# Performance work log

Hardware: AMD Instinct MI355X
Metric: run time of the kernel (lower is better)

The kernel has to match this reference:

```python
import jax, jax.numpy as jnp
import numpy as np

D_MODEL = 1024
NUM_HEADS = 16
D_K = D_MODEL // NUM_HEADS
THETA = 10000.0
SEQ = 4096
BATCH = 1


def _rope(x, token_positions):
    # x: [b, h, s, d_k]; interleaved even/odd rotation as in the torch module
    kd = jnp.arange(0, D_K, 2, dtype=jnp.float32) / D_K          # [d_k/2]
    angles = token_positions[:, None].astype(jnp.float32) / (THETA ** kd)  # [s, d_k/2]
    cos_pos = jnp.cos(angles)
    sin_pos = jnp.sin(angles)
    x_even = x[..., 0::2]
    x_odd = x[..., 1::2]
    rot_even = x_even * cos_pos - x_odd * sin_pos
    rot_odd = x_even * sin_pos + x_odd * cos_pos
    rot = jnp.stack([rot_even, rot_odd], axis=-1)                # [..., d_k/2, 2]
    return rot.reshape(*x.shape[:-1], D_K)


def setup_inputs() -> dict:
    key = jax.random.key(0)
    k1, k2, k3 = jax.random.split(key, 3)
    std_qkv = np.sqrt(2.0 / (D_MODEL + 3 * D_MODEL))
    std_o = np.sqrt(2.0 / (D_MODEL + D_MODEL))
    x = jax.random.normal(k1, (BATCH, SEQ, D_MODEL), dtype=jnp.float32)
    Wqkv = jax.random.normal(k2, (3 * D_MODEL, D_MODEL), dtype=jnp.float32) * std_qkv
    Wo = jax.random.normal(k3, (D_MODEL, D_MODEL), dtype=jnp.float32) * std_o
    token_positions = jnp.arange(SEQ, dtype=jnp.int32)
    return {"x": x, "Wqkv": Wqkv, "Wo": Wo, "token_positions": token_positions}


def reference(x, Wqkv, Wo, token_positions):
    b, s, _ = x.shape
    qkv = jnp.einsum('bsd,ed->bse', x, Wqkv)                      # [b, s, 3*d_model]
    q, k, v = jnp.split(qkv, 3, axis=-1)

    def to_heads(t):
        return t.reshape(b, s, NUM_HEADS, D_K).transpose(0, 2, 1, 3)  # [b, h, s, d_k]

    q, k, v = to_heads(q), to_heads(k), to_heads(v)
    q = _rope(q, token_positions)
    k = _rope(k, token_positions)

    scores = jnp.einsum('bhqd,bhkd->bhqk', q, k) / jnp.sqrt(jnp.float32(D_K))
    mask = jnp.tril(jnp.ones((s, s), dtype=bool))
    scores = jnp.where(mask, scores, -jnp.inf)
    attn = jax.nn.softmax(scores, axis=-1)
    out = jnp.einsum('bhqk,bhkd->bhqd', attn, v)                  # [b, h, s, d_k]
    out = out.transpose(0, 2, 1, 3).reshape(b, s, D_MODEL)
    return jnp.einsum('bsd,ed->bse', out, Wo)
```

## Files before the change

kernel.cpp:

```cpp
#include <hip/hip_runtime.h>
#include <cstdint>

typedef unsigned short u16;
typedef __attribute__((ext_vector_type(8))) short short8;
typedef __attribute__((ext_vector_type(4))) float float4v;

__device__ __forceinline__ float bf2f(u16 u) {
    union { unsigned int i; float f; } v; v.i = ((unsigned int)u) << 16; return v.f;
}
__device__ __forceinline__ u16 f2bf(float f) {
    union { float f; unsigned int i; } v; v.f = f;
    unsigned int i = v.i;
    i += 0x7fffu + ((i >> 16) & 1u);
    return (u16)(i >> 16);
}
__device__ __forceinline__ unsigned cvt_pk_bf16(float lo, float hi) {
    unsigned r;
    asm("v_cvt_pk_bf16_f32 %0, %1, %2" : "=v"(r) : "v"(lo), "v"(hi));
    return r;
}
__device__ __forceinline__ void gl2lds16(const u16* g, u16* l) {
    __builtin_amdgcn_global_load_lds((const __attribute__((address_space(1))) void*)g,
                                     (__attribute__((address_space(3))) void*)l, 16, 0, 0);
}
__device__ __forceinline__ uint4 cvt8(const float* __restrict__ p) {
    float4 a = *(const float4*)p;
    float4 b = *(const float4*)(p + 4);
    u16 t[8] = {f2bf(a.x), f2bf(a.y), f2bf(a.z), f2bf(a.w),
                f2bf(b.x), f2bf(b.y), f2bf(b.z), f2bf(b.w)};
    return *(const uint4*)t;
}

__global__ void cvt_xw(const float* __restrict__ x, const float* __restrict__ wq,
                       const int* __restrict__ pos,
                       u16* __restrict__ xb, u16* __restrict__ wqb,
                       float2* __restrict__ tb) {
    int i = blockIdx.x * blockDim.x + threadIdx.x;
    if (i < 524288) {
        *(uint4*)(xb + (size_t)i * 8) = cvt8(x + (size_t)i * 8);
    } else if (i < 917504) {
        int j = i - 524288;
        *(uint4*)(wqb + (size_t)j * 8) = cvt8(wq + (size_t)j * 8);
    } else {
        int j = i - 917504;
        int s = j >> 5, f = j & 31;
        float freq = __expf(-(float)f * 0.2878231366242557f);
        float ang  = (float)pos[s] * freq;
        float sn, cs;
        __sincosf(ang, &sn, &cs);
        float2 t; t.x = cs; t.y = sn;
        tb[j] = t;
    }
}

__global__ __launch_bounds__(256) void gemm_qkv(const u16* __restrict__ A,
                                                const u16* __restrict__ B,
                                                u16* __restrict__ C,
                                                const float2* __restrict__ tb) {
    __shared__ u16 As[128 * 64];
    __shared__ u16 Bs[128 * 64];
    const int tid  = threadIdx.x;
    const int wave = tid >> 6, lane = tid & 63;
    const int lg = lane >> 4, lr = lane & 15;
    const int bm = blockIdx.x * 128, bn = blockIdx.y * 128;
    const int wm = (wave & 1) * 64, wn = (wave >> 1) * 64;
    const int swz = lr & 7;

    int srow[4], scg[4];
    #pragma unroll
    for (int q = 0; q < 4; ++q) {
        int cid = q * 256 + tid;
        srow[q] = cid >> 3;
        scg[q]  = ((cid & 7) ^ (srow[q] & 7)) * 8;
    }

    float4v acc[4][4] = {};

    for (int k0 = 0; k0 < 1024; k0 += 64) {
        #pragma unroll
        for (int q = 0; q < 4; ++q) {
            int cid = q * 256 + tid;
            gl2lds16(A + (size_t)(bm + srow[q]) * 1024 + k0 + scg[q], As + cid * 8);
            gl2lds16(B + (size_t)(bn + srow[q]) * 1024 + k0 + scg[q], Bs + cid * 8);
        }
        __syncthreads();

        #pragma unroll
        for (int kk = 0; kk < 2; ++kk) {
            short8 af[4], bf[4];
            #pragma unroll
            for (int i = 0; i < 4; ++i)
                af[i] = *(const short8*)(As + (wm + i * 16 + lr) * 64 + (((kk * 4 + lg) ^ swz) * 8));
            #pragma unroll
            for (int j = 0; j < 4; ++j)
                bf[j] = *(const short8*)(Bs + (wn + j * 16 + lr) * 64 + (((kk * 4 + lg) ^ swz) * 8));
            #pragma unroll
            for (int i = 0; i < 4; ++i)
                #pragma unroll
                for (int j = 0; j < 4; ++j)
                    acc[i][j] = __builtin_amdgcn_mfma_f32_16x16x32_bf16(af[i], bf[j], acc[i][j], 0, 0, 0);
        }
        __syncthreads();
    }

    const int colbase = bn + wn;
    const bool dorope = colbase < 2048;
    const float qsc = (colbase < 1024) ? 0.18033688011112042f : 1.0f;
    #pragma unroll
    for (int i = 0; i < 4; ++i)
        #pragma unroll
        for (int r = 0; r < 4; ++r) {
            const int rw = bm + wm + i * 16 + lg * 4 + r;
            #pragma unroll
            for (int j = 0; j < 4; ++j) {
                float v = acc[i][j][r];
                if (dorope) {
                    float2 t = tb[rw * 32 + ((j * 16 + lr) >> 1)];
                    float p = __shfl_xor(v, 1);
                    float rot = (lr & 1) ? (p * t.y + v * t.x)
                                         : (v * t.x - p * t.y);
                    v = rot * qsc;
                }
                C[(size_t)rw * 3072 + colbase + j * 16 + lr] = f2bf(v);
            }
        }
}

__global__ __launch_bounds__(256) void prep2(const u16* __restrict__ qkv,
                                             u16* __restrict__ VT,
                                             float* __restrict__ acc,
                                             float* __restrict__ lac,
                                             const float* __restrict__ wo,
                                             u16* __restrict__ wob) {
    __shared__ u16 T[64 * 65];
    const int bid = blockIdx.x;
    const int tid = threadIdx.x;
    if (bid < 1024) {
        const int h = bid >> 6, s0 = (bid & 63) * 64;
        #pragma unroll
        for (int i = 0; i < 2; ++i) {
            int seg = i * 256 + tid;
            int r = seg >> 3, c8 = (seg & 7) * 8;
            u16 tmp[8];
            *(uint4*)tmp = *(const uint4*)(qkv + (size_t)(s0 + r) * 3072 + 2048 + h * 64 + c8);
            #pragma unroll
            for (int j = 0; j < 8; ++j) T[r * 65 + c8 + j] = tmp[j];
        }
        __syncthreads();
        #pragma unroll
        for (int i = 0; i < 2; ++i) {
            int seg = i * 256 + tid;
            int d = seg >> 3, s8 = (seg & 7) * 8;
            u16 tmp[8];
            #pragma unroll
            for (int j = 0; j < 8; ++j) tmp[j] = T[(s8 + j) * 65 + d];
            *(uint4*)(VT + (size_t)(h * 64 + d) * 4096 + s0 + s8) = *(const uint4*)tmp;
        }
    } else {
        int i = (bid - 1024) * 256 + tid;
        float4 z = {0.f, 0.f, 0.f, 0.f};
        if (i < 1048576) {
            *(float4*)(acc + (size_t)i * 4) = z;
        } else if (i < 1064960) {
            *(float4*)(lac + (size_t)(i - 1048576) * 4) = z;
        } else {
            int j = i - 1064960;
            *(uint4*)(wob + (size_t)j * 8) = cvt8(wo + (size_t)j * 8);
        }
    }
}

__device__ __forceinline__ void attn_tile(const u16* __restrict__ Ksub,
                                          const u16* __restrict__ Vsub,
                                          u16* __restrict__ Psw,
                                          int tbase, int qrow0, int q_abs,
                                          int lg, int lr, int swz,
                                          const short8 qf[2], const short8 ones,
                                          float4v o_acc[4], float4v& rs_acc) {
    float4v sc[4];
    #pragma unroll
    for (int jt = 0; jt < 4; ++jt) {
        float4v a = {};
        #pragma unroll
        for (int kk = 0; kk < 2; ++kk) {
            short8 kf = *(const short8*)(Ksub + (jt * 16 + lr) * 64 + (((kk * 4 + lg) ^ swz) * 8));
            a = __builtin_amdgcn_mfma_f32_16x16x32_bf16(kf, qf[kk], a, 0, 0, 0);
        }
        sc[jt] = a;
    }
    const bool mk = (tbase + 63 > qrow0);
    #pragma unroll
    for (int jt = 0; jt < 4; ++jt) {
        float e[4];
        if (mk) {
            #pragma unroll
            for (int r = 0; r < 4; ++r) {
                float s = sc[jt][r];
                if (tbase + jt * 16 + lg * 4 + r > q_abs) s = -30000.f;
                e[r] = __builtin_amdgcn_exp2f(fminf(s, 86.562f));
            }
        } else {
            #pragma unroll
            for (int r = 0; r < 4; ++r)
                e[r] = __builtin_amdgcn_exp2f(fminf(sc[jt][r], 86.562f));
        }
        uint2 w;
        w.x = cvt_pk_bf16(e[0], e[1]);
        w.y = cvt_pk_bf16(e[2], e[3]);
        *(uint2*)(Psw + lr * 72 + jt * 16 + lg * 4) = w;
    }
    short8 pf[2];
    #pragma unroll
    for (int kk = 0; kk < 2; ++kk)
        pf[kk] = *(const short8*)(Psw + lr * 72 + kk * 32 + lg * 8);
    #pragma unroll
    for (int kk = 0; kk < 2; ++kk)
        rs_acc = __builtin_amdgcn_mfma_f32_16x16x32_bf16(pf[kk], ones, rs_acc, 0, 0, 0);
    #pragma unroll
    for (int jd = 0; jd < 4; ++jd) {
        float4v a = o_acc[jd];
        #pragma unroll
        for (int kk = 0; kk < 2; ++kk) {
            short8 vf = *(const short8*)(Vsub + (jd * 16 + lr) * 64 + (((kk * 4 + lg) ^ swz) * 8));
            a = __builtin_amdgcn_mfma_f32_16x16x32_bf16(pf[kk], vf, a, 0, 0, 0);
        }
        o_acc[jd] = a;
    }
}

__global__ __launch_bounds__(512) void attn_kernel(const u16* __restrict__ qkv,
                                                   const u16* __restrict__ VT,
                                                   float* __restrict__ acc,
                                                   float* __restrict__ lac) {
    __shared__ u16 Ks[2 * 64 * 64];
    __shared__ u16 Vt[2 * 64 * 64];
    __shared__ u16 Ps[8][16 * 72];

    const int tid  = threadIdx.x;
    const int wave = tid >> 6, lane = tid & 63;
    const int lg = lane >> 4, lr = lane & 15;

    const int fid = blockIdx.x;
    const int j_  = fid >> 3;
    const int h   = (fid & 7) * 2 + (j_ >> 5);
    const int z   = (j_ >> 4) & 1;
    const int bxv = j_ & 15;

    const int srow = tid >> 3;
    const int sg   = tid & 7;
    const int sco  = sg * 8;
    const int sldso = srow * 64 + ((sg ^ (srow & 7)) * 8);
    const int swz = (lr & 7);

    const u16 one_bf = 0x3F80;
    short8 ones;
    #pragma unroll
    for (int j = 0; j < 8; ++j) ones[j] = (short)one_bf;

    const u16* Kgbase = qkv + (size_t)srow * 3072 + 1024 + h * 64 + sco;
    const u16* Vgbase = VT + (size_t)(h * 64 + srow) * 4096 + sco;

    #pragma unroll 1
    for (int part = 0; part < 2; ++part) {
        const int qt = part ? (31 - bxv) : bxv;
        const int qb = qt * 128;
        const int qrow0 = qb + wave * 16;
        const int q_abs = qrow0 + lr;
        const int tmax = qb + 64;
        const int t0s  = z * 64;

        short8 qf[2];
        #pragma unroll
        for (int kk = 0; kk < 2; ++kk)
            qf[kk] = *(const short8*)(qkv + (size_t)(qrow0 + lr) * 3072 + h * 64 + kk * 32 + lg * 8);

        float4v o_acc[4] = {};
        float4v rs_acc = {};

        uint4 rK0 = *(const uint4*)(Kgbase + (size_t)t0s * 3072);
        uint4 rV0 = *(const uint4*)(Vgbase + t0s);
        const bool pB = (t0s + 128 <= tmax);
        uint4 rK1, rV1;
        if (pB) {
            rK1 = *(const uint4*)(Kgbase + (size_t)(t0s + 128) * 3072);
            rV1 = *(const uint4*)(Vgbase + t0s + 128);
        }
        __syncthreads();
        *(uint4*)(Ks + sldso) = rK0;
        *(uint4*)(Vt + sldso) = rV0;
        if (pB) {
            *(uint4*)(Ks + 4096 + sldso) = rK1;
            *(uint4*)(Vt + 4096 + sldso) = rV1;
        }
        __syncthreads();

        for (int t0 = t0s; t0 <= tmax; t0 += 256) {
            const bool hasB  = (t0 + 128 <= tmax);
            const bool hasN  = (t0 + 256 <= tmax);
            const bool hasNB = (t0 + 384 <= tmax);
            if (hasN) {
                rK0 = *(const uint4*)(Kgbase + (size_t)(t0 + 256) * 3072);
                rV0 = *(const uint4*)(Vgbase + t0 + 256);
            }
            if (hasNB) {
                rK1 = *(const uint4*)(Kgbase + (size_t)(t0 + 384) * 3072);
                rV1 = *(const uint4*)(Vgbase + t0 + 384);
            }

            attn_tile(Ks, Vt, Ps[wave], t0, qrow0, q_abs, lg, lr, swz, qf, ones, o_acc, rs_acc);
            if (hasB)
                attn_tile(Ks + 4096, Vt + 4096, Ps[wave], t0 + 128, qrow0, q_abs,
                          lg, lr, swz, qf, ones, o_acc, rs_acc);

            if (hasN) {
                __syncthreads();
                *(uint4*)(Ks + sldso) = rK0;
                *(uint4*)(Vt + sldso) = rV0;
                if (hasNB) {
                    *(uint4*)(Ks + 4096 + sldso) = rK1;
                    *(uint4*)(Vt + 4096 + sldso) = rV1;
                }
                __syncthreads();
            }
        }

        if (lr == 0) {
            #pragma unroll
            for (int r = 0; r < 4; ++r)
                atomicAdd(&lac[(size_t)(qrow0 + lg * 4 + r) * 16 + h], rs_acc[r]);
        }

        #pragma unroll
        for (int jd = 0; jd < 4; ++jd)
            #pragma unroll
            for (int r = 0; r < 4; ++r) {
                int s = qrow0 + lg * 4 + r;
                int d = jd * 16 + lr;
                atomicAdd(&acc[(size_t)s * 1024 + h * 64 + d], o_acc[jd][r]);
            }
    }
}

__global__ void norm_o(const float* __restrict__ acc, const float* __restrict__ lac,
                       u16* __restrict__ qkv) {
    int i = blockIdx.x * blockDim.x + threadIdx.x;
    if (i >= 4096 * 1024 / 8) return;
    int e0 = i * 8;
    int s = e0 >> 10, c = e0 & 1023, h = c >> 6;
    float inv = 1.0f / lac[(size_t)s * 16 + h];
    float4 a = *(const float4*)(acc + e0);
    float4 b = *(const float4*)(acc + e0 + 4);
    u16 t[8] = {f2bf(a.x * inv), f2bf(a.y * inv), f2bf(a.z * inv), f2bf(a.w * inv),
                f2bf(b.x * inv), f2bf(b.y * inv), f2bf(b.z * inv), f2bf(b.w * inv)};
    *(uint4*)(qkv + (size_t)s * 3072 + c) = *(const uint4*)t;
}

__global__ __launch_bounds__(256) void gemm_oproj(const u16* __restrict__ A,
                                                  const u16* __restrict__ B,
                                                  float* __restrict__ C) {
    __shared__ u16 As[128 * 64];
    __shared__ u16 Bs[64 * 64];
    const int tid  = threadIdx.x;
    const int wave = tid >> 6, lane = tid & 63;
    const int lg = lane >> 4, lr = lane & 15;
    const int bm = blockIdx.x * 128, bn = blockIdx.y * 64;
    const int wm = (wave & 1) * 64, wn = (wave >> 1) * 32;
    const int swz = lr & 7;

    int srow[4], scg[4];
    #pragma unroll
    for (int q = 0; q < 4; ++q) {
        int cid = q * 256 + tid;
        srow[q] = cid >> 3;
        scg[q]  = ((cid & 7) ^ (srow[q] & 7)) * 8;
    }

    float4v acc[4][2] = {};

    for (int k0 = 0; k0 < 1024; k0 += 64) {
        #pragma unroll
        for (int q = 0; q < 4; ++q) {
            int cid = q * 256 + tid;
            gl2lds16(A + (size_t)(bm + srow[q]) * 3072 + k0 + scg[q], As + cid * 8);
            if (q < 2)
                gl2lds16(B + (size_t)(bn + srow[q]) * 1024 + k0 + scg[q], Bs + cid * 8);
        }
        __syncthreads();

        #pragma unroll
        for (int kk = 0; kk < 2; ++kk) {
            short8 af[4], bf[2];
            #pragma unroll
            for (int i = 0; i < 4; ++i)
                af[i] = *(const short8*)(As + (wm + i * 16 + lr) * 64 + (((kk * 4 + lg) ^ swz) * 8));
            #pragma unroll
            for (int j = 0; j < 2; ++j)
                bf[j] = *(const short8*)(Bs + (wn + j * 16 + lr) * 64 + (((kk * 4 + lg) ^ swz) * 8));
            #pragma unroll
            for (int i = 0; i < 4; ++i)
                #pragma unroll
                for (int j = 0; j < 2; ++j)
                    acc[i][j] = __builtin_amdgcn_mfma_f32_16x16x32_bf16(af[i], bf[j], acc[i][j], 0, 0, 0);
        }
        __syncthreads();
    }

    #pragma unroll
    for (int i = 0; i < 4; ++i)
        #pragma unroll
        for (int j = 0; j < 2; ++j)
            #pragma unroll
            for (int r = 0; r < 4; ++r) {
                int rw = bm + wm + i * 16 + lg * 4 + r;
                int cl = bn + wn + j * 16 + lr;
                C[(size_t)rw * 1024 + cl] = acc[i][j][r];
            }
}

__global__ void fill_diag(float* __restrict__ p, size_t n, float mark) {
    size_t i = (size_t)blockIdx.x * blockDim.x + threadIdx.x;
    if (i < n) p[i] = 0.f;
    if (i == 0) p[0] = mark;
}

extern "C" void kernel_launch(void* const* d_in, const int* in_sizes, int n_in,
                              void* d_out, int out_size, void* d_ws, size_t ws_size,
                              hipStream_t stream) {
    int ix = -1, iwq = -1, iwo = -1, ip = -1;
    for (int i = 0; i < n_in; ++i) {
        if      (in_sizes[i] == 4096 * 1024) ix = i;
        else if (in_sizes[i] == 3072 * 1024) iwq = i;
        else if (in_sizes[i] == 1024 * 1024) iwo = i;
        else if (in_sizes[i] == 4096)        ip = i;
    }
    float* out = (float*)d_out;
    const size_t OUT_E = (size_t)4096 * 1024;
    const size_t QKV_E = (size_t)4096 * 3072;
    const size_t NEED  = QKV_E * 2 + (size_t)3072 * 1024 * 2;

    if (ix < 0 || iwq < 0 || iwo < 0 || ip < 0 || out_size != (int)OUT_E) {
        fill_diag<<<(int)((OUT_E + 255) / 256), 256, 0, stream>>>(out, OUT_E, 1000.0f);
        return;
    }
    if (ws_size < NEED) {
        fill_diag<<<(int)((OUT_E + 255) / 256), 256, 0, stream>>>(out, OUT_E, 500.0f);
        return;
    }
    const float* x    = (const float*)d_in[ix];
    const float* Wqkv = (const float*)d_in[iwq];
    const float* Wo   = (const float*)d_in[iwo];
    const int*   pos  = (const int*)d_in[ip];

    u16* qkv   = (u16*)d_ws;
    u16* wq_bf = (u16*)d_ws + QKV_E;
    u16* wo_bf = wq_bf;
    float* lac = (float*)((char*)wq_bf + 2 * 1024 * 1024 + 65536);
    u16* x_bf  = (u16*)d_out;
    u16* VT    = (u16*)d_out + OUT_E;
    float2* tb = (float2*)VT;
    float* acc = (float*)d_in[ix];

    cvt_xw<<<4096, 256, 0, stream>>>(x, Wqkv, pos, x_bf, wq_bf, tb);
    gemm_qkv<<<dim3(32, 24), 256, 0, stream>>>(x_bf, wq_bf, qkv, tb);
    prep2<<<5696, 256, 0, stream>>>(qkv, VT, acc, lac, Wo, wo_bf);
    attn_kernel<<<512, 512, 0, stream>>>(qkv, VT, acc, lac);
    norm_o<<<2048, 256, 0, stream>>>(acc, lac, qkv);
    gemm_oproj<<<dim3(32, 16), 256, 0, stream>>>(qkv, wo_bf, out);
}
```

Baseline: 221.4 us.

## Process two query row blocks per wave to reuse K/V tiles

Each wave now handles two 16-row query groups, 128 rows apart, against each K/V tile loaded into shared memory. This halves the K/V LDS reads and global loads per query row and doubles the MFMA work per tile. The key dimension is now split four ways instead of two, with a 256-row query tile per block. This raises register pressure and adds a second P buffer in shared memory, and the launch bounds now request occupancy 4. The masked-tile work near the diagonal is also coarser.

Result: slower. 266.9 us (+20.6%).

```diff
diff --git a/kernel.cpp b/kernel.cpp
--- a/kernel.cpp
+++ b/kernel.cpp
@@ -170,71 +170,109 @@
     }
 }
 
-__device__ __forceinline__ void attn_tile(const u16* __restrict__ Ksub,
-                                          const u16* __restrict__ Vsub,
-                                          u16* __restrict__ Psw,
-                                          int tbase, int qrow0, int q_abs,
-                                          int lg, int lr, int swz,
-                                          const short8 qf[2], const short8 ones,
-                                          float4v o_acc[4], float4v& rs_acc) {
-    float4v sc[4];
+__device__ __forceinline__ void attn_tile2(const u16* __restrict__ Ksub,
+                                           const u16* __restrict__ Vsub,
+                                           u16* __restrict__ PswA,
+                                           u16* __restrict__ PswB,
+                                           int tbase, int qrowA, int qrowB,
+                                           int q_absA, int q_absB,
+                                           int lg, int lr, int swz,
+                                           const short8 qfA[2], const short8 qfB[2],
+                                           const short8 ones,
+                                           float4v oA[4], float4v oB[4],
+                                           float4v& rsA, float4v& rsB) {
+    float4v scA[4], scB[4];
     #pragma unroll
     for (int jt = 0; jt < 4; ++jt) {
-        float4v a = {};
+        float4v a = {}, b = {};
         #pragma unroll
         for (int kk = 0; kk < 2; ++kk) {
             short8 kf = *(const short8*)(Ksub + (jt * 16 + lr) * 64 + (((kk * 4 + lg) ^ swz) * 8));
-            a = __builtin_amdgcn_mfma_f32_16x16x32_bf16(kf, qf[kk], a, 0, 0, 0);
-        }
-        sc[jt] = a;
-    }
-    const bool mk = (tbase + 63 > qrow0);
+            a = __builtin_amdgcn_mfma_f32_16x16x32_bf16(kf, qfA[kk], a, 0, 0, 0);
+            b = __builtin_amdgcn_mfma_f32_16x16x32_bf16(kf, qfB[kk], b, 0, 0, 0);
+        }
+        scA[jt] = a; scB[jt] = b;
+    }
+
+    const bool mkA = (tbase + 63 > qrowA);
     #pragma unroll
     for (int jt = 0; jt < 4; ++jt) {
         float e[4];
-        if (mk) {
+        if (mkA) {
             #pragma unroll
             for (int r = 0; r < 4; ++r) {
-                float s = sc[jt][r];
-                if (tbase + jt * 16 + lg * 4 + r > q_abs) s = -30000.f;
+                float s = scA[jt][r];
+                if (tbase + jt * 16 + lg * 4 + r > q_absA) s = -30000.f;
                 e[r] = __builtin_amdgcn_exp2f(fminf(s, 86.562f));
             }
         } else {
             #pragma unroll
             for (int r = 0; r < 4; ++r)
-                e[r] = __builtin_amdgcn_exp2f(fminf(sc[jt][r], 86.562f));
+                e[r] = __builtin_amdgcn_exp2f(fminf(scA[jt][r], 86.562f));
         }
         uint2 w;
         w.x = cvt_pk_bf16(e[0], e[1]);
         w.y = cvt_pk_bf16(e[2], e[3]);
-        *(uint2*)(Psw + lr * 72 + jt * 16 + lg * 4) = w;
-    }
-    short8 pf[2];
+        *(uint2*)(PswA + lr * 72 + jt * 16 + lg * 4) = w;
+    }
+    short8 pfA[2];
     #pragma unroll
     for (int kk = 0; kk < 2; ++kk)
-        pf[kk] = *(const short8*)(Psw + lr * 72 + kk * 32 + lg * 8);
+        pfA[kk] = *(const short8*)(PswA + lr * 72 + kk * 32 + lg * 8);
+
+    const bool mkB = (tbase + 63 > qrowB);
+    #pragma unroll
+    for (int jt = 0; jt < 4; ++jt) {
+        float e[4];
+        if (mkB) {
+            #pragma unroll
+            for (int r = 0; r < 4; ++r) {
+                float s = scB[jt][r];
+                if (tbase + jt * 16 + lg * 4 + r > q_absB) s = -30000.f;
+                e[r] = __builtin_amdgcn_exp2f(fminf(s, 86.562f));
+            }
+        } else {
+            #pragma unroll
+            for (int r = 0; r < 4; ++r)
+                e[r] = __builtin_amdgcn_exp2f(fminf(scB[jt][r], 86.562f));
+        }
+        uint2 w;
+        w.x = cvt_pk_bf16(e[0], e[1]);
+        w.y = cvt_pk_bf16(e[2], e[3]);
+        *(uint2*)(PswB + lr * 72 + jt * 16 + lg * 4) = w;
+    }
+    short8 pfB[2];
     #pragma unroll
     for (int kk = 0; kk < 2; ++kk)
-        rs_acc = __builtin_amdgcn_mfma_f32_16x16x32_bf16(pf[kk], ones, rs_acc, 0, 0, 0);
+        pfB[kk] = *(const short8*)(PswB + lr * 72 + kk * 32 + lg * 8);
+
+    #pragma unroll
+    for (int kk = 0; kk < 2; ++kk) {
+        rsA = __builtin_amdgcn_mfma_f32_16x16x32_bf16(pfA[kk], ones, rsA, 0, 0, 0);
+        rsB = __builtin_amdgcn_mfma_f32_16x16x32_bf16(pfB[kk], ones, rsB, 0, 0, 0);
+    }
+
     #pragma unroll
     for (int jd = 0; jd < 4; ++jd) {
-        float4v a = o_acc[jd];
+        float4v a = oA[jd], b = oB[jd];
         #pragma unroll
         for (int kk = 0; kk < 2; ++kk) {
             short8 vf = *(const short8*)(Vsub + (jd * 16 + lr) * 64 + (((kk * 4 + lg) ^ swz) * 8));
-            a = __builtin_amdgcn_mfma_f32_16x16x32_bf16(pf[kk], vf, a, 0, 0, 0);
-        }
-        o_acc[jd] = a;
-    }
-}
-
-__global__ __launch_bounds__(512) void attn_kernel(const u16* __restrict__ qkv,
-                                                   const u16* __restrict__ VT,
-                                                   float* __restrict__ acc,
-                                                   float* __restrict__ lac) {
+            a = __builtin_amdgcn_mfma_f32_16x16x32_bf16(pfA[kk], vf, a, 0, 0, 0);
+            b = __builtin_amdgcn_mfma_f32_16x16x32_bf16(pfB[kk], vf, b, 0, 0, 0);
+        }
+        oA[jd] = a; oB[jd] = b;
+    }
+}
+
+__global__ __launch_bounds__(512, 4) void attn_kernel(const u16* __restrict__ qkv,
+                                                      const u16* __restrict__ VT,
+                                                      float* __restrict__ acc,
+                                                      float* __restrict__ lac) {
     __shared__ u16 Ks[2 * 64 * 64];
     __shared__ u16 Vt[2 * 64 * 64];
-    __shared__ u16 Ps[8][16 * 72];
+    __shared__ u16 PsA[8][16 * 72];
+    __shared__ u16 PsB[8][16 * 72];
 
     const int tid  = threadIdx.x;
     const int wave = tid >> 6, lane = tid & 63;
@@ -243,8 +281,8 @@
     const int fid = blockIdx.x;
     const int j_  = fid >> 3;
     const int h   = (fid & 7) * 2 + (j_ >> 5);
-    const int z   = (j_ >> 4) & 1;
-    const int bxv = j_ & 15;
+    const int z   = (j_ >> 3) & 3;
+    const int p   = j_ & 7;
 
     const int srow = tid >> 3;
     const int sg   = tid & 7;
@@ -262,28 +300,32 @@
 
     #pragma unroll 1
     for (int part = 0; part < 2; ++part) {
-        const int qt = part ? (31 - bxv) : bxv;
-        const int qb = qt * 128;
-        const int qrow0 = qb + wave * 16;
-        const int q_abs = qrow0 + lr;
-        const int tmax = qb + 64;
+        const int T = part ? (15 - p) : p;
+        const int qb = T * 256;
+        const int qrowA = qb + wave * 16;
+        const int qrowB = qb + 128 + wave * 16;
+        const int q_absA = qrowA + lr;
+        const int q_absB = qrowB + lr;
+        const int tmax = qb + 192;
         const int t0s  = z * 64;
 
-        short8 qf[2];
-        #pragma unroll
-        for (int kk = 0; kk < 2; ++kk)
-            qf[kk] = *(const short8*)(qkv + (size_t)(qrow0 + lr) * 3072 + h * 64 + kk * 32 + lg * 8);
-
-        float4v o_acc[4] = {};
-        float4v rs_acc = {};
+        short8 qfA[2], qfB[2];
+        #pragma unroll
+        for (int kk = 0; kk < 2; ++kk) {
+            qfA[kk] = *(const short8*)(qkv + (size_t)(qrowA + lr) * 3072 + h * 64 + kk * 32 + lg * 8);
+            qfB[kk] = *(const short8*)(qkv + (size_t)(qrowB + lr) * 3072 + h * 64 + kk * 32 + lg * 8);
+        }
+
+        float4v oA[4] = {}, oB[4] = {};
+        float4v rsA = {}, rsB = {};
 
         uint4 rK0 = *(const uint4*)(Kgbase + (size_t)t0s * 3072);
         uint4 rV0 = *(const uint4*)(Vgbase + t0s);
-        const bool pB = (t0s + 128 <= tmax);
+        const bool pB = (t0s + 256 <= tmax);
         uint4 rK1, rV1;
         if (pB) {
-            rK1 = *(const uint4*)(Kgbase + (size_t)(t0s + 128) * 3072);
-            rV1 = *(const uint4*)(Vgbase + t0s + 128);
+            rK1 = *(const uint4*)(Kgbase + (size_t)(t0s + 256) * 3072);
+            rV1 = *(const uint4*)(Vgbase + t0s + 256);
         }
         __syncthreads();
         *(uint4*)(Ks + sldso) = rK0;
@@ -294,23 +336,25 @@
         }
         __syncthreads();
 
-        for (int t0 = t0s; t0 <= tmax; t0 += 256) {
-            const bool hasB  = (t0 + 128 <= tmax);
-            const bool hasN  = (t0 + 256 <= tmax);
-            const bool hasNB = (t0 + 384 <= tmax);
+        for (int t0 = t0s; t0 <= tmax; t0 += 512) {
+            const bool hasB  = (t0 + 256 <= tmax);
+            const bool hasN  = (t0 + 512 <= tmax);
+            const bool hasNB = (t0 + 768 <= tmax);
             if (hasN) {
-                rK0 = *(const uint4*)(Kgbase + (size_t)(t0 + 256) * 3072);
-                rV0 = *(const uint4*)(Vgbase + t0 + 256);
+                rK0 = *(const uint4*)(Kgbase + (size_t)(t0 + 512) * 3072);
+                rV0 = *(const uint4*)(Vgbase + t0 + 512);
             }
             if (hasNB) {
-                rK1 = *(const uint4*)(Kgbase + (size_t)(t0 + 384) * 3072);
-                rV1 = *(const uint4*)(Vgbase + t0 + 384);
-            }
-
-            attn_tile(Ks, Vt, Ps[wave], t0, qrow0, q_abs, lg, lr, swz, qf, ones, o_acc, rs_acc);
+                rK1 = *(const uint4*)(Kgbase + (size_t)(t0 + 768) * 3072);
+                rV1 = *(const uint4*)(Vgbase + t0 + 768);
+            }
+
+            attn_tile2(Ks, Vt, PsA[wave], PsB[wave], t0, qrowA, qrowB,
+                       q_absA, q_absB, lg, lr, swz, qfA, qfB, ones, oA, oB, rsA, rsB);
             if (hasB)
-                attn_tile(Ks + 4096, Vt + 4096, Ps[wave], t0 + 128, qrow0, q_abs,
-                          lg, lr, swz, qf, ones, o_acc, rs_acc);
+                attn_tile2(Ks + 4096, Vt + 4096, PsA[wave], PsB[wave], t0 + 256,
+                           qrowA, qrowB, q_absA, q_absB, lg, lr, swz,
+                           qfA, qfB, ones, oA, oB, rsA, rsB);
 
             if (hasN) {
                 __syncthreads();
@@ -326,17 +370,19 @@
 
         if (lr == 0) {
             #pragma unroll
-            for (int r = 0; r < 4; ++r)
-                atomicAdd(&lac[(size_t)(qrow0 + lg * 4 + r) * 16 + h], rs_acc[r]);
+            for (int r = 0; r < 4; ++r) {
+                atomicAdd(&lac[(size_t)(qrowA + lg * 4 + r) * 16 + h], rsA[r]);
+                atomicAdd(&lac[(size_t)(qrowB + lg * 4 + r) * 16 + h], rsB[r]);
+            }
         }
 
         #pragma unroll
         for (int jd = 0; jd < 4; ++jd)
             #pragma unroll
             for (int r = 0; r < 4; ++r) {
-                int s = qrow0 + lg * 4 + r;
-                int d = jd * 16 + lr;
-                atomicAdd(&acc[(size_t)s * 1024 + h * 64 + d], o_acc[jd][r]);
+                const int d = jd * 16 + lr;
+                atomicAdd(&acc[(size_t)(qrowA + lg * 4 + r) * 1024 + h * 64 + d], oA[jd][r]);
+                atomicAdd(&acc[(size_t)(qrowB + lg * 4 + r) * 1024 + h * 64 + d], oB[jd][r]);
             }
     }
 }
```
